# Performance work log

Measured on AMD Instinct MI355X. Metric: run time of the kernel, lower is better.

Reference implementation:

```python
import jax, jax.numpy as jnp
import numpy as np

NUM_ENTITIES = 50000
NUM_RELATIONS = 500
DIM = 100
BATCH = 16
EPS = 1e-5  # torch BatchNorm1d default eps


def _bn2(x, gamma, beta):
    # train-mode BatchNorm1d on (B, d): stats over batch axis
    mean = jnp.mean(x, axis=0, keepdims=True)
    var = jnp.var(x, axis=0, keepdims=True)
    return (x - mean) * jax.lax.rsqrt(var + EPS) * gamma + beta


def _bn3(x, gamma, beta):
    # train-mode BatchNorm1d on (B, d, N): stats over (batch, length)
    mean = jnp.mean(x, axis=(0, 2), keepdims=True)
    var = jnp.var(x, axis=(0, 2), keepdims=True)
    return (x - mean) * jax.lax.rsqrt(var + EPS) * gamma[None, :, None] + beta[None, :, None]


def _cmul(a, b):
    return (a[0] * b[0] - a[1] * b[1], a[0] * b[1] + a[1] * b[0])


def _cadd(a, b):
    return (a[0] + b[0], a[1] + b[1])


def _cdiv(a, b):
    den = b[0] * b[0] + b[1] * b[1]
    return ((a[0] * b[0] + a[1] * b[1]) / den, (a[1] * b[0] - a[0] * b[1]) / den)


def setup_inputs() -> dict:
    key = jax.random.key(0)
    ks = jax.random.split(key, 12)
    d = DIM
    inp = {
        "h_idx": jax.random.randint(ks[0], (BATCH,), 0, NUM_ENTITIES),
        "r_idx": jax.random.randint(ks[1], (BATCH,), 0, NUM_RELATIONS),
        # ComplexEmbedding E (real, imag)
        "E_a": jax.random.normal(ks[2], (NUM_ENTITIES, d), jnp.float32) * 0.1,
        "E_b": jax.random.normal(ks[3], (NUM_ENTITIES, d), jnp.float32) * 0.1,
        # MobiusEmbedding R: 4 complex coefficients (a,b,c,d), real/imag parts
        "R_re": jax.random.normal(ks[4], (NUM_RELATIONS, 4, d), jnp.float32) * 0.1,
        "R_im": jax.random.normal(ks[5], (NUM_RELATIONS, 4, d), jnp.float32) * 0.1,
        # plain relation embedding feeding the Tucker cores
        "R2": jax.random.normal(ks[6], (NUM_RELATIONS, d), jnp.float32) * 0.1,
        # Tucker cores (relation_dim, entity_dim, entity_dim)
        "W_re": jax.random.uniform(ks[7], (d, d, d), jnp.float32, -0.1, 0.1),
        "W_im": jax.random.uniform(ks[8], (d, d, d), jnp.float32, -0.1, 0.1),
    }
    # BatchNorm affine params (bn0/bn1 of each CoreTuckER, and complex E_bn)
    gk = jax.random.split(ks[9], 6)
    bk = jax.random.split(ks[10], 6)
    names = ["g0r", "g1r", "g0i", "g1i", "gEa", "gEb"]
    bnames = ["b0r", "b1r", "b0i", "b1i", "bEa", "bEb"]
    for i, (gn, bn) in enumerate(zip(names, bnames)):
        inp[gn] = 1.0 + 0.05 * jax.random.normal(gk[i], (d,), jnp.float32)
        inp[bn] = 0.05 * jax.random.normal(bk[i], (d,), jnp.float32)
    return inp


def _forward(h_idx, r_idx, E_a, E_b, R_re, R_im, R2, W_re, W_im,
             g0r, b0r, g1r, b1r, g0i, b0i, g1i, b1i, gEa, bEa, gEb, bEb):
    h_a = E_a[h_idx]            # (B, d)
    h_b = E_b[h_idx]
    r2 = R2[r_idx]              # (B, d)

    # relation-specific Tucker maps W_mat = r2 . W  -> (B, d, d)
    Wm_re = jnp.einsum("bk,kef->bef", r2, W_re)
    Wm_im = jnp.einsum("bk,kef->bef", r2, W_im)

    def core(h, Wm, g0, b0, g1, b1):
        x = _bn2(h, g0, b0)
        x = jnp.einsum("be,bef->bf", x, Wm)  # (B,1,d) bmm (B,d,d)
        return _bn2(x, g1, b1)

    t_a = core(h_a, Wm_re, g0r, b0r, g1r, b1r)
    t_b = core(h_b, Wm_im, g0i, b0i, g1i, b1i)

    # Mobius multiplication: (h*r_a + r_b) / (h*r_c + r_d)
    rr = R_re[r_idx]            # (B, 4, d)
    ri = R_im[r_idx]
    h = (t_a, t_b)
    r_a = (rr[:, 0], ri[:, 0]); r_b = (rr[:, 1], ri[:, 1])
    r_c = (rr[:, 2], ri[:, 2]); r_d = (rr[:, 3], ri[:, 3])
    top = _cadd(_cmul(h, r_a), r_b)
    bot = _cadd(_cmul(h, r_c), r_d)
    t = _cdiv(top, bot)         # complex pair, each (B, d)

    # transform ALL entities with the same relation-specific Tucker map
    # CoreTuckER.w: (B,e,f) x (N,e) -> (B, f, N)
    Ea_t = jnp.einsum("bef,ne->bfn", Wm_re, E_a)
    Eb_t = jnp.einsum("bef,ne->bfn", Wm_im, E_b)
    # ComplexBatchNorm1d on (B, d, N); dropout is identity in eval mode
    Ea_t = _bn3(Ea_t, gEa, bEa)
    Eb_t = _bn3(Eb_t, gEb, bEb)

    # BatchComplexScoringAll: (B,1,d) bmm (B,d,N) for each complex part
    score = (jnp.einsum("bf,bfn->bn", t[0], Ea_t)
             + jnp.einsum("bf,bfn->bn", t[1], Eb_t))
    return jax.nn.sigmoid(score)  # (B, N)


def reference(h_idx, r_idx, E_a, E_b, R_re, R_im, R2, W_re, W_im,
              g0r, b0r, g1r, b1r, g0i, b0i, g1i, b1i, gEa, bEa, gEb, bEb):
    return _forward(h_idx, r_idx, E_a, E_b, R_re, R_im, R2, W_re, W_im,
                    g0r, b0r, g1r, b1r, g0i, b0i, g1i, b1i, gEa, bEa, gEb, bEb)
```

## Files before the change

### kernel.cpp

```cpp
#include <hip/hip_runtime.h>
#include <math.h>

#define D100 100
#define NE 50000
#define BATCH 16
#define EPS_F 1e-5f
#define TPT 782
#define TPB2 4
#define NBG 196
#define QCI 20
#define QCB 5
#define QNJ 1664
#define SLICES 16
#define SEG3 13
#define K1B 157

typedef __attribute__((ext_vector_type(8))) short short8;
typedef __attribute__((ext_vector_type(16))) float float16;
typedef unsigned short u16;
typedef unsigned int u32;

__device__ __forceinline__ float bf2f(u16 v) {
  return __uint_as_float(((u32)v) << 16);
}
__device__ __forceinline__ float f4get(const float4& v, int j) {
  switch (j) { case 0: return v.x; case 1: return v.y; case 2: return v.z; default: return v.w; }
}
__device__ __forceinline__ u32 cvt_pk_bf16(float lo, float hi) {
  u32 val;
  asm volatile("v_cvt_pk_bf16_f32 %0, %1, %2" : "=v"(val) : "v"(lo), "v"(hi));
  return val;
}

#define K2F_LOAD(tile)                                          \
    { int n0 = (tile) * 64;                                     \
      _Pragma("unroll")                                         \
      for (int s = 0; s < 4; s++) {                             \
        int i = s * 256 + tid;                                  \
        float4 a = make_float4(0.f, 0.f, 0.f, 0.f);             \
        float4 b = make_float4(0.f, 0.f, 0.f, 0.f);             \
        if (i < 800) {                                          \
          int p = i / 25, e4 = i - p * 25;                      \
          int n = n0 + 2 * p;                                   \
          if (n < NE)     a = E4[(long)n * 25 + e4];            \
          if (n + 1 < NE) b = E4[(long)(n + 1) * 25 + e4];      \
        }                                                       \
        st0[s] = a; st1[s] = b;                                 \
      } }

#define K2F_WRITE()                                             \
    { _Pragma("unroll")                                         \
      for (int s = 0; s < 4; s++) {                             \
        int i = s * 256 + tid;                                  \
        if (i < 800) {                                          \
          int p = i / 25, e4 = i - p * 25;                      \
          int ncl = p >> 3, half = (p >> 2) & 1, elem = 2 * (p & 3); \
          _Pragma("unroll")                                     \
          for (int j = 0; j < 4; j++) {                         \
            int e = e4 * 4 + j;                                 \
            u32 val = cvt_pk_bf16(f4get(st0[s], j), f4get(st1[s], j)); \
            FR32[((e >> 5) * 2048 + ncl * 512 + ((e & 31) + 32 * half) * 8 + elem) >> 1] = val; \
          } } } }

__global__ __launch_bounds__(256) void kA(const float* __restrict__ W_re,
                                          const float* __restrict__ W_im,
                                          const float* __restrict__ R2,
                                          const int* __restrict__ r_idx,
                                          const float* __restrict__ E_a,
                                          const float* __restrict__ E_b,
                                          float* __restrict__ Wm,
                                          float* __restrict__ Gp,
                                          float* __restrict__ CSp) {
  __shared__ union {
    u16 fr[8192];
    struct { float r2s[16][100]; float red[4][64][17]; } k1;
  } sm;
  const int bid = blockIdx.x, tid = threadIdx.x;

  if (bid < 2 * NBG) {
    const int t = bid / NBG, bx = bid - t * NBG;
    const float4* E4 = (const float4*)(t ? E_b : E_a);
    u16* FR = sm.fr;
    u32* FR32 = (u32*)sm.fr;
    const int wave = tid >> 6, lane = tid & 63, l31 = lane & 31;

    for (int i = tid; i < 4096; i += 256) FR32[i] = 0;

    const int ti0 = bx * TPB2;
    const int nt = min(ti0 + TPB2, TPT) - ti0;

    float16 acc0, acc1, acc2, acc3;
#pragma unroll 16
    for (int r = 0; r < 16; r++) { acc0[r] = 0.f; acc1[r] = 0.f; acc2[r] = 0.f; acc3[r] = 0.f; }
    float cs = 0.f;
    float4 st0[4], st1[4];

    __syncthreads();
    K2F_LOAD(ti0);
    K2F_WRITE();
    __syncthreads();

    for (int tt = 0; tt < nt; tt++) {
      if (tt + 1 < nt) K2F_LOAD(ti0 + tt + 1);
#pragma unroll
      for (int ncl = 0; ncl < 4; ncl++) {
        const u16* pf = FR + ncl * 512 + lane * 8;
        short8 f0 = *(const short8*)pf;
        short8 f1 = *(const short8*)(pf + 2048);
        short8 f2 = *(const short8*)(pf + 4096);
        short8 f3 = *(const short8*)(pf + 6144);
        short8 av = *(const short8*)(pf + wave * 2048);
        acc0 = __builtin_amdgcn_mfma_f32_32x32x16_bf16(av, f0, acc0, 0, 0, 0);
        acc1 = __builtin_amdgcn_mfma_f32_32x32x16_bf16(av, f1, acc1, 0, 0, 0);
        acc2 = __builtin_amdgcn_mfma_f32_32x32x16_bf16(av, f2, acc2, 0, 0, 0);
        acc3 = __builtin_amdgcn_mfma_f32_32x32x16_bf16(av, f3, acc3, 0, 0, 0);
#pragma unroll
        for (int j = 0; j < 8; j++) cs += bf2f((u16)av[j]);
      }
      __syncthreads();
      if (tt + 1 < nt) {
        K2F_WRITE();
        __syncthreads();
      }
    }

    float* gp = Gp + ((long)t * NBG + bx) * 10000;
#pragma unroll 16
    for (int r = 0; r < 16; r++) {
      int m = (r & 3) + 8 * (r >> 2) + 4 * (lane >> 5);
      int e = wave * 32 + m;
      if (e < 100) {
        gp[e * 100 + l31] = acc0[r];
        gp[e * 100 + 32 + l31] = acc1[r];
        gp[e * 100 + 64 + l31] = acc2[r];
        if (l31 < 4) gp[e * 100 + 96 + l31] = acc3[r];
      }
    }
    cs += __shfl_xor(cs, 32);
    int row = wave * 32 + l31;
    if (lane < 32 && row < 100)
      CSp[((long)t * NBG + bx) * 100 + row] = cs;
  } else {
    int bid2 = bid - 2 * NBG;
    int t = bid2 / K1B, eb = bid2 - t * K1B;
    const float* W = t ? W_im : W_re;
    const int efl = tid & 63, kg = tid >> 6;
    const int ef = eb * 64 + efl;
    for (int i = tid; i < 1600; i += 256) {
      int b = i / 100, k = i - b * 100;
      sm.k1.r2s[b][k] = R2[r_idx[b] * 100 + k];
    }
    __syncthreads();
    float acc[16];
#pragma unroll
    for (int b = 0; b < 16; b++) acc[b] = 0.f;
    if (ef < 10000) {
      const float* wp = W + (long)kg * 25 * 10000 + ef;
#pragma unroll 5
      for (int kk = 0; kk < 25; kk++) {
        float w = wp[kk * 10000];
        int k = kg * 25 + kk;
#pragma unroll
        for (int b = 0; b < 16; b++) acc[b] = fmaf(sm.k1.r2s[b][k], w, acc[b]);
      }
    }
#pragma unroll
    for (int b = 0; b < 16; b++) sm.k1.red[kg][efl][b] = acc[b];
    __syncthreads();
#pragma unroll
    for (int q = 0; q < 4; q++) {
      int o = tid + 256 * q;
      int b = o >> 6, efl2 = o & 63;
      int ef2 = eb * 64 + efl2;
      if (ef2 < 10000) {
        float s = sm.k1.red[0][efl2][b] + sm.k1.red[1][efl2][b] +
                  sm.k1.red[2][efl2][b] + sm.k1.red[3][efl2][b];
        Wm[t * 160000 + b * 10000 + ef2] = s;
      }
    }
  }
}

__global__ __launch_bounds__(256) void kB(const float* __restrict__ Gp,
                                          const float* __restrict__ CSp,
                                          float* __restrict__ Gp2,
                                          float* __restrict__ CSp2,
                                          const float* __restrict__ E_a,
                                          const float* __restrict__ E_b,
                                          const int* __restrict__ h_idx,
                                          const float* __restrict__ Wm,
                                          const float* __restrict__ g0r, const float* __restrict__ b0r,
                                          const float* __restrict__ g0i, const float* __restrict__ b0i,
                                          float* __restrict__ traw) {
  __shared__ float hrows[1600], x[100];
  const int bid = blockIdx.x, tid = threadIdx.x;
  if (bid < 40 * SLICES * 2) {
    int chunk = bid % 40, slice = (bid / 40) % SLICES, t = bid / (40 * SLICES);
    int nb0 = slice * SEG3;
    int nb1 = min(nb0 + SEG3, NBG);
    int idx = chunk * 256 + tid;
    if (idx < 10000) {
      float s = 0.f;
      const float* p = Gp + ((long)t * NBG + nb0) * 10000 + idx;
      for (int q = nb0; q < nb1; q++, p += 10000) s += *p;
      Gp2[(t * SLICES + slice) * 10000 + idx] = s;
    }
    if (chunk == 0 && tid < 100) {
      float s = 0.f;
      const float* p = CSp + ((long)t * NBG + nb0) * 100 + tid;
      for (int q = nb0; q < nb1; q++, p += 100) s += *p;
      CSp2[(t * SLICES + slice) * 100 + tid] = s;
    }
  } else {
    int bid2 = bid - 40 * SLICES * 2;
    int t = bid2 >> 4, b = bid2 & 15;
    const float4* E4 = (const float4*)(t ? E_b : E_a);
    const float* g0 = t ? g0i : g0r;
    const float* be0 = t ? b0i : b0r;
    for (int i = tid; i < 400; i += 256) {
      int b2 = i / 25, e4 = i - b2 * 25;
      float4 v = E4[(long)h_idx[b2] * 25 + e4];
      *(float4*)&hrows[b2 * 100 + e4 * 4] = v;
    }
    __syncthreads();
    if (tid < 100) {
      float m = 0.f, s = 0.f;
#pragma unroll
      for (int b2 = 0; b2 < 16; b2++) { float v = hrows[b2 * 100 + tid]; m += v; s += v * v; }
      m *= (1.f / 16.f);
      float var = s * (1.f / 16.f) - m * m;
      x[tid] = (hrows[b * 100 + tid] - m) * rsqrtf(var + EPS_F) * g0[tid] + be0[tid];
    }
    __syncthreads();
    if (tid < 100) {
      const float* W = Wm + t * 160000 + b * 10000 + tid;
      float s = 0.f;
#pragma unroll 4
      for (int e = 0; e < 100; e++) s = fmaf(x[e], W[e * 100], s);
      traw[t * 1600 + b * 100 + tid] = s;
    }
  }
}

__global__ __launch_bounds__(128) void kQF(const float* __restrict__ Gp2,
                                           const float* __restrict__ CSp2,
                                           const float* __restrict__ Wm,
                                           float* __restrict__ qf,
                                           float* __restrict__ s2q) {
  const int bid = blockIdx.x;
  const int cx = bid % 13, ci = (bid / 13) % QCB, t = bid / (13 * QCB);
  const int tid = threadIdx.x;
  __shared__ __align__(16) float Gl[QCI][100];
  __shared__ float CSl[QCI];
  for (int i = tid; i < QCI * 100; i += 128) {
    int k = i / 100, e = i - k * 100;
    float s = 0.f;
    const float* p = Gp2 + (long)t * SLICES * 10000 + (ci * QCI + k) * 100 + e;
#pragma unroll
    for (int sl = 0; sl < SLICES; sl++) s += p[sl * 10000];
    Gl[k][e] = s;
  }
  if (tid < QCI) {
    float s = 0.f;
    const float* p = CSp2 + (long)t * SLICES * 100 + ci * QCI + tid;
#pragma unroll
    for (int sl = 0; sl < SLICES; sl++) s += p[sl * 100];
    CSl[tid] = s;
  }
  __syncthreads();
  int j = cx * 128 + tid;
  if (j >= 1600) return;
  int b = j / 100, f = j - b * 100;
  const float* Y = Wm + t * 160000 + b * 10000 + f;
  float yci[QCI];
  float cs2 = 0.f;
#pragma unroll
  for (int k = 0; k < QCI; k++) {
    yci[k] = Y[(ci * QCI + k) * 100];
    cs2 = fmaf(CSl[k], yci[k], cs2);
  }
  float acc = 0.f;
#pragma unroll 5
  for (int e4 = 0; e4 < 25; e4++) {
    float ye0 = Y[(e4 * 4 + 0) * 100];
    float ye1 = Y[(e4 * 4 + 1) * 100];
    float ye2 = Y[(e4 * 4 + 2) * 100];
    float ye3 = Y[(e4 * 4 + 3) * 100];
    float s0 = 0.f, s1 = 0.f, s2 = 0.f, s3 = 0.f;
#pragma unroll
    for (int k = 0; k < QCI; k++) {
      float4 g = *(const float4*)&Gl[k][e4 * 4];
      s0 = fmaf(g.x, yci[k], s0);
      s1 = fmaf(g.y, yci[k], s1);
      s2 = fmaf(g.z, yci[k], s2);
      s3 = fmaf(g.w, yci[k], s3);
    }
    acc += s0 * ye0 + s1 * ye1 + s2 * ye2 + s3 * ye3;
  }
  qf[((long)t * QCB + ci) * QNJ + j] = acc;
  s2q[((long)t * QCB + ci) * QNJ + j] = cs2;
}

__global__ __launch_bounds__(256) void kD(const float* __restrict__ traw,
                                          const int* __restrict__ r_idx,
                                          const float* __restrict__ g1r, const float* __restrict__ b1r,
                                          const float* __restrict__ g1i, const float* __restrict__ b1i,
                                          const float* __restrict__ R_re, const float* __restrict__ R_im,
                                          const float* __restrict__ qf, const float* __restrict__ s2q,
                                          const float* __restrict__ gEa, const float* __restrict__ bEa,
                                          const float* __restrict__ gEb, const float* __restrict__ bEb,
                                          const float* __restrict__ Wm,
                                          float* __restrict__ u, float* __restrict__ c) {
  const int bid = blockIdx.x, tid = threadIdx.x;
  const int t2 = bid >> 4, bo = bid & 15;
  __shared__ float tr[3200], sca[200], shl[200], al[200], be[200];
  __shared__ float w0[100], w1[100], t01l[200], pc[128];
  __shared__ float Wl[10100];
  for (int i = tid; i < 3200; i += 256) tr[i] = traw[i];
  __syncthreads();
  if (tid < 200) {
    int tt = tid / 100, f = tid - tt * 100;
    float m = 0.f, s = 0.f;
#pragma unroll
    for (int b = 0; b < 16; b++) { float v = tr[tt * 1600 + b * 100 + f]; m += v; s += v * v; }
    m *= (1.f / 16.f);
    float var = s * (1.f / 16.f) - m * m;
    float g = tt ? g1i[f] : g1r[f];
    float bb = tt ? b1i[f] : b1r[f];
    float sc = rsqrtf(var + EPS_F) * g;
    sca[tid] = sc; shl[tid] = bb - m * sc;
    float s1 = 0.f, s2 = 0.f;
    const float* q = qf + (long)tt * QCB * QNJ + f;
    const float* z = s2q + (long)tt * QCB * QNJ + f;
#pragma unroll
    for (int ci = 0; ci < QCB; ci++) {
#pragma unroll
      for (int b2 = 0; b2 < 16; b2++) {
        s1 += q[ci * QNJ + b2 * 100];
        s2 += z[ci * QNJ + b2 * 100];
      }
    }
    float mean = s2 * (1.f / 800000.f);
    float var2 = s1 * (1.f / 800000.f) - mean * mean;
    float gE = tt ? gEb[f] : gEa[f];
    float bE = tt ? bEb[f] : bEa[f];
    float aa = rsqrtf(var2 + EPS_F) * gE;
    al[tid] = aa; be[tid] = bE - mean * aa;
  }
  __syncthreads();
  if (tid < 100) {
    int f = tid;
    float va = tr[bo * 100 + f] * sca[f] + shl[f];
    float vb = tr[1600 + bo * 100 + f] * sca[100 + f] + shl[100 + f];
    int base = r_idx[bo] * 400 + f;
    float ra0 = R_re[base],       ra1 = R_im[base];
    float rb0 = R_re[base + 100], rb1 = R_im[base + 100];
    float rc0 = R_re[base + 200], rc1 = R_im[base + 200];
    float rd0 = R_re[base + 300], rd1 = R_im[base + 300];
    float top0 = va * ra0 - vb * ra1 + rb0;
    float top1 = va * ra1 + vb * ra0 + rb1;
    float bot0 = va * rc0 - vb * rc1 + rd0;
    float bot1 = va * rc1 + vb * rc0 + rd1;
    float den = bot0 * bot0 + bot1 * bot1;
    float t0 = (top0 * bot0 + top1 * bot1) / den;
    float t1 = (top1 * bot0 - top0 * bot1) / den;
    t01l[f] = t0; t01l[100 + f] = t1;
    w0[f] = t0 * al[f];
    w1[f] = t1 * al[100 + f];
  }
  if (tid < 128) pc[tid] = 0.f;
  __syncthreads();
  if (tid < 100) pc[tid] = t01l[tid] * be[tid] + t01l[100 + tid] * be[100 + tid];
  __syncthreads();
  for (int o = 64; o > 0; o >>= 1) {
    if (tid < o) pc[tid] += pc[tid + o];
    __syncthreads();
  }
  if (tid == 0 && t2 == 0) c[bo] = pc[0];
  __syncthreads();
  {
    const float4* W4 = (const float4*)(Wm + t2 * 160000 + bo * 10000);
    for (int i = tid; i < 2500; i += 256) {
      float4 v = W4[i];
      int e = (i * 4) / 100, f0 = (i * 4) - e * 100;
      float* dst = &Wl[e * 101 + f0];
      dst[0] = v.x; dst[1] = v.y; dst[2] = v.z; dst[3] = v.w;
    }
    __syncthreads();
    if (tid < 100) {
      const float* row = &Wl[tid * 101];
      const float* w = t2 ? w1 : w0;
      float s = 0.f;
#pragma unroll 4
      for (int f = 0; f < 100; f++) s = fmaf(w[f], row[f], s);
      u[(t2 * 100 + tid) * 16 + bo] = s;
    }
  }
}

__global__ __launch_bounds__(256) void k9_score(const float* __restrict__ E_a,
                                                const float* __restrict__ E_b,
                                                const float* __restrict__ u,
                                                const float* __restrict__ c,
                                                float* __restrict__ out) {
  int n = blockIdx.x * 256 + threadIdx.x;
  if (n >= NE) return;
  const float4* Ea4 = (const float4*)E_a;
  const float4* Eb4 = (const float4*)E_b;
  float acc[16];
#pragma unroll
  for (int b = 0; b < 16; b++) acc[b] = 0.f;
  for (int e4 = 0; e4 < 25; e4++) {
    float4 va = Ea4[n * 25 + e4];
    float4 vb = Eb4[n * 25 + e4];
    const float* ua = u + e4 * 64;
    const float* ub = u + 1600 + e4 * 64;
#pragma unroll
    for (int j = 0; j < 4; j++) {
      float fa = f4get(va, j);
      float fb = f4get(vb, j);
#pragma unroll
      for (int b = 0; b < 16; b++) {
        acc[b] = fmaf(ua[j * 16 + b], fa, acc[b]);
        acc[b] = fmaf(ub[j * 16 + b], fb, acc[b]);
      }
    }
  }
#pragma unroll
  for (int b = 0; b < 16; b++) {
    float x = acc[b] + c[b];
    out[b * NE + n] = 1.f / (1.f + expf(-x));
  }
}

extern "C" void kernel_launch(void* const* d_in, const int* in_sizes, int n_in,
                              void* d_out, int out_size, void* d_ws, size_t ws_size,
                              hipStream_t stream) {
  const int* h_idx = (const int*)d_in[0];
  const int* r_idx = (const int*)d_in[1];
  const float* E_a = (const float*)d_in[2];
  const float* E_b = (const float*)d_in[3];
  const float* R_re = (const float*)d_in[4];
  const float* R_im = (const float*)d_in[5];
  const float* R2 = (const float*)d_in[6];
  const float* W_re = (const float*)d_in[7];
  const float* W_im = (const float*)d_in[8];
  const float* g0r = (const float*)d_in[9];
  const float* b0r = (const float*)d_in[10];
  const float* g1r = (const float*)d_in[11];
  const float* b1r = (const float*)d_in[12];
  const float* g0i = (const float*)d_in[13];
  const float* b0i = (const float*)d_in[14];
  const float* g1i = (const float*)d_in[15];
  const float* b1i = (const float*)d_in[16];
  const float* gEa = (const float*)d_in[17];
  const float* bEa = (const float*)d_in[18];
  const float* gEb = (const float*)d_in[19];
  const float* bEb = (const float*)d_in[20];
  float* out = (float*)d_out;
  float* ws = (float*)d_ws;

  float* Wm = ws;
  float* u = Wm + 320000;
  float* c = u + 3200;
  float* qf = c + 16;
  float* s2q = qf + 16640;
  float* traw = s2q + 16640;
  float* Gp = traw + 3200;
  float* CSp = Gp + (long)2 * NBG * 10000;
  float* Gp2 = CSp + (long)2 * NBG * 100;
  float* CSp2 = Gp2 + 320000;

  hipLaunchKernelGGL(kA, dim3(2 * NBG + 2 * K1B), dim3(256), 0, stream,
                     W_re, W_im, R2, r_idx, E_a, E_b, Wm, Gp, CSp);
  hipLaunchKernelGGL(kB, dim3(40 * SLICES * 2 + 32), dim3(256), 0, stream,
                     Gp, CSp, Gp2, CSp2, E_a, E_b, h_idx, Wm,
                     g0r, b0r, g0i, b0i, traw);
  hipLaunchKernelGGL(kQF, dim3(13 * QCB * 2), dim3(128), 0, stream,
                     Gp2, CSp2, Wm, qf, s2q);
  hipLaunchKernelGGL(kD, dim3(32), dim3(256), 0, stream, traw, r_idx,
                     g1r, b1r, g1i, b1i, R_re, R_im, qf, s2q,
                     gEa, bEa, gEb, bEb, Wm, u, c);
  hipLaunchKernelGGL(k9_score, dim3((NE + 255) / 256), dim3(256), 0, stream,
                     E_a, E_b, u, c, out);
}
```

Baseline: 82.12 us.

## Swizzle LDS fragment layout in kA and split score kernel over real/imag halves

The kA staging buffer is changed to an XOR-swizzled u32 layout, so MFMA operand reads from different row blocks fall on different LDS banks. Writes and reads use the matching swizzle. The k9_score kernel now assigns the real and imaginary embedding parts to separate halves of each block and combines the partial sums through shared memory. This doubles the thread count per entity and is meant to raise parallelism and memory-level concurrency, at the cost of an extra LDS round trip and a barrier.

```diff
diff --git a/kernel.cpp b/kernel.cpp
--- a/kernel.cpp
+++ b/kernel.cpp
@@ -54,12 +54,14 @@
         int i = s * 256 + tid;                                  \
         if (i < 800) {                                          \
           int p = i / 25, e4 = i - p * 25;                      \
-          int ncl = p >> 3, half = (p >> 2) & 1, elem = 2 * (p & 3); \
+          int ncl = p >> 3, half = (p >> 2) & 1, elem2 = p & 3; \
           _Pragma("unroll")                                     \
           for (int j = 0; j < 4; j++) {                         \
             int e = e4 * 4 + j;                                 \
+            int rb = e >> 5;                                    \
+            int slot = (e & 31) + 32 * half;                    \
             u32 val = cvt_pk_bf16(f4get(st0[s], j), f4get(st1[s], j)); \
-            FR32[((e >> 5) * 2048 + ncl * 512 + ((e & 31) + 32 * half) * 8 + elem) >> 1] = val; \
+            FR32[rb * 1024 + ncl * 256 + (((slot << 2) + elem2) ^ (rb << 2))] = val; \
           } } } }
 
 __global__ __launch_bounds__(256) void kA(const float* __restrict__ W_re,
@@ -72,7 +74,7 @@
                                           float* __restrict__ Gp,
                                           float* __restrict__ CSp) {
   __shared__ union {
-    u16 fr[8192];
+    u32 fr32[4096];
     struct { float r2s[16][100]; float red[4][64][17]; } k1;
   } sm;
   const int bid = blockIdx.x, tid = threadIdx.x;
@@ -80,8 +82,7 @@
   if (bid < 2 * NBG) {
     const int t = bid / NBG, bx = bid - t * NBG;
     const float4* E4 = (const float4*)(t ? E_b : E_a);
-    u16* FR = sm.fr;
-    u32* FR32 = (u32*)sm.fr;
+    u32* FR32 = sm.fr32;
     const int wave = tid >> 6, lane = tid & 63, l31 = lane & 31;
 
     for (int i = tid; i < 4096; i += 256) FR32[i] = 0;
@@ -95,6 +96,8 @@
     float cs = 0.f;
     float4 st0[4], st1[4];
 
+    const int lx = lane << 2;
+
     __syncthreads();
     K2F_LOAD(ti0);
     K2F_WRITE();
@@ -104,12 +107,12 @@
       if (tt + 1 < nt) K2F_LOAD(ti0 + tt + 1);
 #pragma unroll
       for (int ncl = 0; ncl < 4; ncl++) {
-        const u16* pf = FR + ncl * 512 + lane * 8;
-        short8 f0 = *(const short8*)pf;
-        short8 f1 = *(const short8*)(pf + 2048);
-        short8 f2 = *(const short8*)(pf + 4096);
-        short8 f3 = *(const short8*)(pf + 6144);
-        short8 av = *(const short8*)(pf + wave * 2048);
+        const u32* reg = FR32 + ncl * 256;
+        short8 f0 = *(const short8*)(reg + 0 * 1024 + (lx ^ 0));
+        short8 f1 = *(const short8*)(reg + 1 * 1024 + (lx ^ 4));
+        short8 f2 = *(const short8*)(reg + 2 * 1024 + (lx ^ 8));
+        short8 f3 = *(const short8*)(reg + 3 * 1024 + (lx ^ 12));
+        short8 av = *(const short8*)(reg + wave * 1024 + (lx ^ (wave << 2)));
         acc0 = __builtin_amdgcn_mfma_f32_32x32x16_bf16(av, f0, acc0, 0, 0, 0);
         acc1 = __builtin_amdgcn_mfma_f32_32x32x16_bf16(av, f1, acc1, 0, 0, 0);
         acc2 = __builtin_amdgcn_mfma_f32_32x32x16_bf16(av, f2, acc2, 0, 0, 0);
@@ -403,33 +406,40 @@
                                                 const float* __restrict__ u,
                                                 const float* __restrict__ c,
                                                 float* __restrict__ out) {
-  int n = blockIdx.x * 256 + threadIdx.x;
-  if (n >= NE) return;
-  const float4* Ea4 = (const float4*)E_a;
-  const float4* Eb4 = (const float4*)E_b;
+  __shared__ float ps[2][128][17];
+  const int tid = threadIdx.x;
+  const int t = tid >> 7, nl = tid & 127;
+  const int n = blockIdx.x * 128 + nl;
   float acc[16];
 #pragma unroll
   for (int b = 0; b < 16; b++) acc[b] = 0.f;
-  for (int e4 = 0; e4 < 25; e4++) {
-    float4 va = Ea4[n * 25 + e4];
-    float4 vb = Eb4[n * 25 + e4];
-    const float* ua = u + e4 * 64;
-    const float* ub = u + 1600 + e4 * 64;
-#pragma unroll
-    for (int j = 0; j < 4; j++) {
-      float fa = f4get(va, j);
-      float fb = f4get(vb, j);
+  if (n < NE) {
+    const float4* Et4 = (const float4*)(t ? E_b : E_a);
+    const float* ut = u + t * 1600;
+    for (int e4 = 0; e4 < 25; e4++) {
+      float4 v = Et4[(long)n * 25 + e4];
+      const float* uu = ut + e4 * 64;
+#pragma unroll
+      for (int j = 0; j < 4; j++) {
+        float fv = f4get(v, j);
+#pragma unroll
+        for (int b = 0; b < 16; b++)
+          acc[b] = fmaf(uu[j * 16 + b], fv, acc[b]);
+      }
+    }
+  }
+#pragma unroll
+  for (int b = 0; b < 16; b++) ps[t][nl][b] = acc[b];
+  __syncthreads();
+  if (tid < 128) {
+    int n2 = blockIdx.x * 128 + tid;
+    if (n2 < NE) {
 #pragma unroll
       for (int b = 0; b < 16; b++) {
-        acc[b] = fmaf(ua[j * 16 + b], fa, acc[b]);
-        acc[b] = fmaf(ub[j * 16 + b], fb, acc[b]);
-      }
-    }
-  }
-#pragma unroll
-  for (int b = 0; b < 16; b++) {
-    float x = acc[b] + c[b];
-    out[b * NE + n] = 1.f / (1.f + expf(-x));
+        float x = ps[0][tid][b] + ps[1][tid][b] + c[b];
+        out[b * NE + n2] = 1.f / (1.f + expf(-x));
+      }
+    }
   }
 }
 
@@ -481,6 +491,6 @@
   hipLaunchKernelGGL(kD, dim3(32), dim3(256), 0, stream, traw, r_idx,
                      g1r, b1r, g1i, b1i, R_re, R_im, qf, s2q,
                      gEa, bEa, gEb, bEb, Wm, u, c);
-  hipLaunchKernelGGL(k9_score, dim3((NE + 255) / 256), dim3(256), 0, stream,
+  hipLaunchKernelGGL(k9_score, dim3((NE + 127) / 128), dim3(256), 0, stream,
                      E_a, E_b, u, c, out);
 }
```

New measurement: 95.81 us. +16.7%, slower.
